# Optimization experiments

Measured on AMD Instinct MI355X. Metric: run time of the kernel, lower is better.

The kernel has to match this reference:

```python
import jax, jax.numpy as jnp
import numpy as np

NUM_HEADS = 8
POOL = 4  # kq_downscale kernel/stride (spatial)
B, S, H, W, C = 32, 8, 32, 32, 128
TOTAL_KEY_DEPTH = 512
VAL_FILTERS = 128
OUT_FILTERS = 64


def _avg_pool(x):
    # tf.nn.avg_pool3d with kernel/stride [1,1,4,4,1], SAME padding (dims divide evenly)
    win = (1, 1, POOL, POOL, 1)
    s = jax.lax.reduce_window(x, 0.0, jax.lax.add, win, win, 'SAME')
    return s / (POOL * POOL)


def _conv2d(x, w, b):
    # TimeDistributed Conv2D, same padding. x: (B,S,H,W,Cin), w: (kh,kw,Cin,Cout)
    Bx, Sx, Hx, Wx, Cx = x.shape
    y = jax.lax.conv_general_dilated(
        x.reshape(Bx * Sx, Hx, Wx, Cx), w, (1, 1), 'SAME',
        dimension_numbers=('NHWC', 'HWIO', 'NHWC'))
    return y.reshape(Bx, Sx, Hx, Wx, -1) + b


def _rel_emb(length_q, length_k, max_rel, table):
    # _generate_relative_positions_embeddings
    rk = jnp.arange(length_k)
    rq = rk[-length_q:]
    idx = jnp.clip(rk[None, :] - rq[:, None], -max_rel, max_rel) + max_rel
    return table[idx]  # (Lq, Lk, depth)


def setup_inputs() -> dict:
    key = jax.random.key(0)
    ks = jax.random.split(key, 11)
    qk_in = (H // POOL) * (W // POOL) * C          # 8*8*128 = 8192
    d_vh = H * W * VAL_FILTERS // NUM_HEADS         # 16384 per-head value depth
    d_kh = TOTAL_KEY_DEPTH // NUM_HEADS             # 64
    return {
        'inputs': jax.random.normal(ks[0], (B, 1, H, W, C), jnp.float32),
        'k_antecedent': jax.random.normal(ks[1], (B, S, H, W, C), jnp.float32),
        'v_antecedent': jax.random.normal(ks[2], (B, S, H, W, C), jnp.float32),
        'w_q': jax.random.normal(ks[3], (qk_in, TOTAL_KEY_DEPTH), jnp.float32) * 0.02,
        'w_k': jax.random.normal(ks[4], (qk_in, TOTAL_KEY_DEPTH), jnp.float32) * 0.02,
        'conv_v_w': jax.random.normal(ks[5], (3, 3, C, VAL_FILTERS), jnp.float32) * 0.02,
        'conv_v_b': jnp.zeros((VAL_FILTERS,), jnp.float32),
        'conv_o_w': jax.random.normal(ks[6], (3, 3, VAL_FILTERS, OUT_FILTERS), jnp.float32) * 0.02,
        'conv_o_b': jnp.zeros((OUT_FILTERS,), jnp.float32),
        'table_k': jax.random.normal(ks[7], (S, d_kh), jnp.float32) * 0.05,
        'table_v': jax.random.normal(ks[8], (S, d_vh), jnp.float32) * 0.05,
    }


def reference(inputs, k_antecedent, v_antecedent, w_q, w_k,
              conv_v_w, conv_v_b, conv_o_w, conv_o_b, table_k, table_v):
    Bx, Sx, Hx, Wx, Cx = v_antecedent.shape
    nh = NUM_HEADS
    max_rel = Sx // 2 - 1  # attn_factor_reduc/2 - 1

    # downscale + flatten q/k antecedents
    q_a = _avg_pool(inputs).reshape(Bx, 1, -1)
    k_a = _avg_pool(k_antecedent).reshape(Bx, Sx, -1)
    q = q_a @ w_q                   # (B,1,Dk)
    k = k_a @ w_k                   # (B,S,Dk)
    v = _conv2d(v_antecedent, conv_v_w, conv_v_b).reshape(Bx, Sx, -1)  # (B,S,Dv)

    def split(x):  # (B,L,D) -> (B,h,L,D/h)
        Bz, L, D = x.shape
        return x.reshape(Bz, L, nh, D // nh).transpose(0, 2, 1, 3)

    q, k, v = split(q), split(k), split(v)
    q = q * (q.shape[-1] ** -0.5)

    # relative-position logits: _relative_attention_inner(q, k, z_k, transpose=True)
    z_k = _rel_emb(1, Sx, max_rel, table_k)  # (1,S,dkh)
    logits = jnp.einsum('bhqd,bhkd->bhqk', q, k) + jnp.einsum('bhqd,qkd->bhqk', q, z_k)
    weights = jax.nn.softmax(logits, axis=-1)  # (B,h,1,S)

    # relative values: _relative_attention_inner(weights, v, z_v, transpose=False)
    z_v = _rel_emb(1, Sx, max_rel, table_v)  # (1,S,dvh)
    x = jnp.einsum('bhqk,bhkd->bhqd', weights, v) + jnp.einsum('bhqk,qkd->bhqd', weights, z_v)

    # combine heads, restore spatial shape, output conv
    x = x.transpose(0, 2, 1, 3).reshape(Bx, 1, Hx, Wx, -1)  # (B,1,H,W,Fv)
    out = _conv2d(x, conv_o_w, conv_o_b)                     # (B,1,H,W,Fo)
    return out
```

## Files before the change

### kernel.cpp

```cpp
#include <hip/hip_runtime.h>
#include <hip/hip_bf16.h>

typedef __hip_bfloat16 bf16;
typedef __attribute__((ext_vector_type(8))) short bf16x8;
typedef __attribute__((ext_vector_type(4))) float f32x4;

constexpr int B_ = 32, S_ = 8, H_ = 32, W_ = 32, C_ = 128;
constexpr int NH_ = 8, KD_ = 512, DKH_ = 64, VF_ = 128, OF_ = 64;
constexpr int QKIN_ = 8192;

static __device__ __forceinline__ short bfbits(float f) {
    bf16 h = __float2bfloat16(f);
    short s;
    __builtin_memcpy(&s, &h, 2);
    return s;
}
static __device__ __forceinline__ unsigned int packbf2(float a, float b) {
    return ((unsigned int)(unsigned short)bfbits(b) << 16) | (unsigned short)bfbits(a);
}


static __device__ __forceinline__ void dev_pool4(const float* __restrict__ in,
                                                 short* __restrict__ out, int idx) {
    int c4 = (idx & 31) * 4;
    int pw = (idx >> 5) & 7;
    int ph = (idx >> 8) & 7;
    int img = idx >> 11;
    const float* p = in + (((size_t)img * H_ + ph * 4) * W_ + pw * 4) * C_ + c4;
    float4 s = {0.f, 0.f, 0.f, 0.f};
#pragma unroll
    for (int half = 0; half < 2; ++half) {
        float4 v[8];
#pragma unroll
        for (int j = 0; j < 8; ++j) {
            int dy = half * 2 + (j >> 2), dx = j & 3;
            v[j] = *reinterpret_cast<const float4*>(p + (dy * W_ + dx) * C_);
        }
#pragma unroll
        for (int j = 0; j < 8; ++j) {
            s.x += v[j].x; s.y += v[j].y; s.z += v[j].z; s.w += v[j].w;
        }
    }
    uint2 pk;
    pk.x = packbf2(s.x * 0.0625f, s.y * 0.0625f);
    pk.y = packbf2(s.z * 0.0625f, s.w * 0.0625f);
    *reinterpret_cast<uint2*>(out + (size_t)img * QKIN_ + (ph * 8 + pw) * 128 + c4) = pk;
}

static __device__ __forceinline__ void dev_wT(const float* __restrict__ w,
                                              short* __restrict__ wT, int local,
                                              float (*t)[65]) {
    int k0 = (local >> 3) * 64, n0 = (local & 7) * 64;
    int c4 = (threadIdx.x & 15) * 4, r16 = threadIdx.x >> 4;
#pragma unroll
    for (int i = 0; i < 4; ++i) {
        int kr = i * 16 + r16;
        float4 v = *reinterpret_cast<const float4*>(
            w + (size_t)(k0 + kr) * KD_ + n0 + c4);
        t[kr][c4 + 0] = v.x;
        t[kr][c4 + 1] = v.y;
        t[kr][c4 + 2] = v.z;
        t[kr][c4 + 3] = v.w;
    }
    __syncthreads();
    int n = threadIdx.x >> 3, kg = threadIdx.x & 7;
#pragma unroll
    for (int half = 0; half < 2; ++half) {
        int nn = n + half * 32;
        short v[8];
#pragma unroll
        for (int j = 0; j < 8; ++j) v[j] = bfbits(t[kg * 8 + j][nn]);
        *reinterpret_cast<bf16x8*>(wT + (size_t)(n0 + nn) * QKIN_ + k0 + kg * 8) =
            *reinterpret_cast<bf16x8*>(v);
    }
}

static __device__ __forceinline__ void dev_wtrans(const float* __restrict__ in,
                                                  short* __restrict__ out, int idx,
                                                  int CO) {
    int tap = idx / (128 * CO);
    int rem = idx % (128 * CO);
    int co = rem / 128;
    int ci = rem & 127;
    out[idx] = bfbits(in[((size_t)tap * 128 + ci) * CO + co]);
}

constexpr int PB_ZERO  = 144;
constexpr int PB_POOLI = PB_ZERO + 256;
constexpr int PB_POOLK = PB_POOLI + 2048;
constexpr int PB_WTQ   = PB_POOLK + 1024;
constexpr int PB_WTK   = PB_WTQ + 1024;
constexpr int PB_WV    = PB_WTK + 576;
constexpr int PB_WO    = PB_WV + 288;

__global__ __launch_bounds__(256) void k_prep(
    const float* __restrict__ inp, const float* __restrict__ k_ant,
    const float* __restrict__ w_q, const float* __restrict__ w_k,
    const float* __restrict__ cvw, const float* __restrict__ cow,
    float* __restrict__ qk_zero, short* __restrict__ q_a, short* __restrict__ k_a,
    short* __restrict__ wqT, short* __restrict__ wkT,
    short* __restrict__ wvT, short* __restrict__ woT) {
    __shared__ float t[64][65];
    int bx = blockIdx.x;
    if (bx < PB_ZERO) {
        int i = (bx * 256 + threadIdx.x) * 4;
        float4 z = {0.f, 0.f, 0.f, 0.f};
        *reinterpret_cast<float4*>(qk_zero + i) = z;
    } else if (bx < PB_POOLI) {
        dev_pool4(inp, q_a, (bx - PB_ZERO) * 256 + threadIdx.x);
    } else if (bx < PB_POOLK) {
        dev_pool4(k_ant, k_a, (bx - PB_POOLI) * 256 + threadIdx.x);
    } else if (bx < PB_WTK) {
        if (bx < PB_WTQ)
            dev_wT(w_q, wqT, bx - PB_POOLK, t);
        else
            dev_wT(w_k, wkT, bx - PB_WTQ, t);
    } else if (bx < PB_WV) {
        dev_wtrans(cvw, wvT, (bx - PB_WTK) * 256 + threadIdx.x, 128);
    } else {
        dev_wtrans(cow, woT, (bx - PB_WV) * 256 + threadIdx.x, 64);
    }
}

__global__ __launch_bounds__(256) void k_gemm2(
    const short* __restrict__ qa, const short* __restrict__ ka,
    const short* __restrict__ wqTp, const short* __restrict__ wkTp,
    float* __restrict__ qo, float* __restrict__ ko) {
    int wave = threadIdx.x >> 6, lane = threadIdx.x & 63;
    int quad = lane >> 4, l15 = lane & 15;
    int id = blockIdx.x;
    const short* A;
    const short* WT;
    float* out;
    int m0, rem;
    if (id < 64) {
        A = qa; WT = wqTp; out = qo; m0 = 0; rem = id;
    } else {
        id -= 64;
        A = ka; WT = wkTp; out = ko;
        m0 = (id >> 6) * 32; rem = id & 63;
    }
    int n0 = (rem & 3) * 128 + wave * 32;
    int k0 = (rem >> 2) * 512;
    f32x4 acc[2][2];
#pragma unroll
    for (int mt = 0; mt < 2; ++mt)
#pragma unroll
        for (int nt = 0; nt < 2; ++nt) acc[mt][nt] = (f32x4){0.f, 0.f, 0.f, 0.f};
    const short* a0p = A + (size_t)(m0 + l15) * QKIN_;
    const short* a1p = a0p + 16 * QKIN_;
    const short* b0p = WT + (size_t)(n0 + l15) * QKIN_;
    const short* b1p = b0p + 16 * QKIN_;
    for (int kk = k0 + quad * 8; kk < k0 + 512; kk += 32) {
        bf16x8 a0 = *reinterpret_cast<const bf16x8*>(a0p + kk);
        bf16x8 a1 = *reinterpret_cast<const bf16x8*>(a1p + kk);
        bf16x8 b0 = *reinterpret_cast<const bf16x8*>(b0p + kk);
        bf16x8 b1 = *reinterpret_cast<const bf16x8*>(b1p + kk);
        acc[0][0] = __builtin_amdgcn_mfma_f32_16x16x32_bf16(a0, b0, acc[0][0], 0, 0, 0);
        acc[0][1] = __builtin_amdgcn_mfma_f32_16x16x32_bf16(a0, b1, acc[0][1], 0, 0, 0);
        acc[1][0] = __builtin_amdgcn_mfma_f32_16x16x32_bf16(a1, b0, acc[1][0], 0, 0, 0);
        acc[1][1] = __builtin_amdgcn_mfma_f32_16x16x32_bf16(a1, b1, acc[1][1], 0, 0, 0);
    }
#pragma unroll
    for (int mt = 0; mt < 2; ++mt)
#pragma unroll
        for (int nt = 0; nt < 2; ++nt)
#pragma unroll
            for (int reg = 0; reg < 4; ++reg)
                atomicAdd(&out[(size_t)(m0 + mt * 16 + quad * 4 + reg) * KD_ +
                               n0 + nt * 16 + l15],
                          acc[mt][nt][reg]);
}

static __device__ __forceinline__ void dev_softmax(
    const float* __restrict__ q, const float* __restrict__ kmat,
    const float* __restrict__ tbk, int b, int h, float* w8s) {
    if (threadIdx.x < 64) {
        int d = threadIdx.x;
        float qv = q[(size_t)b * KD_ + h * DKH_ + d];
        float lg[8];
        float m = -1e30f;
#pragma unroll
        for (int s = 0; s < 8; ++s) {
            int zi = (s < 4) ? 0 : (s - 4);
            float kv = kmat[((size_t)b * S_ + s) * KD_ + h * DKH_ + d] + tbk[zi * DKH_ + d];
            float p = qv * kv * 0.125f;
#pragma unroll
            for (int msk = 1; msk < 64; msk <<= 1) p += __shfl_xor(p, msk);
            lg[s] = p;
            m = fmaxf(m, p);
        }
        float sum = 0.f;
#pragma unroll
        for (int s = 0; s < 8; ++s) {
            lg[s] = expf(lg[s] - m);
            sum += lg[s];
        }
        if (d == 0) {
            float inv = 1.f / sum;
#pragma unroll
            for (int s = 0; s < 8; ++s) w8s[s] = lg[s] * inv;
        }
    }
}

__global__ __launch_bounds__(256) void k_mix(
    const float* __restrict__ v_ant, const float* __restrict__ q,
    const float* __restrict__ kmat, const float* __restrict__ tbk,
    short* __restrict__ xmix) {
    __shared__ float w8s[8];
    int bx = blockIdx.x;
    int b = bx / 48;
    int rem6 = bx % 48;
    int h = rem6 / 6, r = rem6 % 6;
    dev_softmax(q, kmat, tbk, b, h, w8s);
    __syncthreads();
    int yimg = 4 * h - 1 + r;
    short* outp = xmix + ((size_t)(b * 8 + h) * 6 + r) * 4096;
    if (yimg < 0 || yimg >= H_) {
        uint2 z = {0u, 0u};
#pragma unroll
        for (int it = 0; it < 4; ++it) {
            int off = (it * 256 + threadIdx.x) * 4;
            *reinterpret_cast<uint2*>(outp + off) = z;
        }
        return;
    }
    float w8[8];
#pragma unroll
    for (int s = 0; s < 8; ++s) w8[s] = w8s[s];
    const float* base0 = v_ant + (size_t)b * 1048576 + yimg * 4096;
#pragma unroll
    for (int it = 0; it < 4; ++it) {
        int off = (it * 256 + threadIdx.x) * 4;
        float4 v[8];
#pragma unroll
        for (int s = 0; s < 8; ++s)
            v[s] = *reinterpret_cast<const float4*>(base0 + (size_t)s * 131072 + off);
        float4 a = {0.f, 0.f, 0.f, 0.f};
#pragma unroll
        for (int s = 0; s < 8; ++s) {
            a.x = fmaf(w8[s], v[s].x, a.x);
            a.y = fmaf(w8[s], v[s].y, a.y);
            a.z = fmaf(w8[s], v[s].z, a.z);
            a.w = fmaf(w8[s], v[s].w, a.w);
        }
        uint2 pk;
        pk.x = packbf2(a.x, a.y);
        pk.y = packbf2(a.z, a.w);
        *reinterpret_cast<uint2*>(outp + off) = pk;
    }
}

static __device__ __forceinline__ void dev_stage_copy(const short* __restrict__ src,
                                                      short* __restrict__ strip) {
    for (int i = threadIdx.x; i < 384; i += 256) {
        int r = i >> 6, remz = i & 63;
        int side = remz >> 5, cg = remz & 31;
        uint2 z = {0u, 0u};
        *reinterpret_cast<uint2*>(&strip[(r * 34 + side * 33) * 136 + cg * 4]) = z;
    }
#pragma unroll
    for (int round = 0; round < 3; ++round) {
        uint2 vv[8];
#pragma unroll
        for (int j = 0; j < 8; ++j) {
            int i = (round * 8 + j) * 256 + threadIdx.x;
            vv[j] = *reinterpret_cast<const uint2*>(src + i * 4);
        }
#pragma unroll
        for (int j = 0; j < 8; ++j) {
            int i = (round * 8 + j) * 256 + threadIdx.x;
            int r = i >> 10, rem = i & 1023;
            int px = rem >> 5, cg = rem & 31;
            *reinterpret_cast<uint2*>(&strip[(r * 34 + px + 1) * 136 + cg * 4]) = vv[j];
        }
    }
}

static __device__ __forceinline__ void dev_stage6(const short* __restrict__ src,
                                                  int y0, short* __restrict__ strip) {
    for (int i = threadIdx.x; i < 384; i += 256) {
        int r = i >> 6, remz = i & 63;
        int side = remz >> 5, cg = remz & 31;
        uint2 z = {0u, 0u};
        *reinterpret_cast<uint2*>(&strip[(r * 34 + side * 33) * 136 + cg * 4]) = z;
    }
#pragma unroll
    for (int round = 0; round < 3; ++round) {
        uint2 vv[8];
#pragma unroll
        for (int j = 0; j < 8; ++j) {
            int i = (round * 8 + j) * 256 + threadIdx.x;
            int r = i >> 10, rem = i & 1023;
            int yimg = y0 - 1 + r;
            vv[j] = (uint2){0u, 0u};
            if (0 <= yimg && yimg < H_)
                vv[j] = *reinterpret_cast<const uint2*>(src + yimg * 4096 + rem * 4);
        }
#pragma unroll
        for (int j = 0; j < 8; ++j) {
            int i = (round * 8 + j) * 256 + threadIdx.x;
            int r = i >> 10, rem = i & 1023;
            int px = rem >> 5, cg = rem & 31;
            *reinterpret_cast<uint2*>(&strip[(r * 34 + px + 1) * 136 + cg * 4]) = vv[j];
        }
    }
}

__global__ __launch_bounds__(256) void k_convv2(
    const short* __restrict__ xmix, const short* __restrict__ wvT,
    const float* __restrict__ bias, const float* __restrict__ tbv,
    const float* __restrict__ q, const float* __restrict__ kmat,
    const float* __restrict__ tbk, short* __restrict__ x) {
    __shared__ short strip[6 * 34 * 136];
    __shared__ float w8s[8];
    int b = blockIdx.x >> 3, h = blockIdx.x & 7;
    int y0 = 4 * h;
    dev_softmax(q, kmat, tbk, b, h, w8s);
    dev_stage_copy(xmix + (size_t)(b * 8 + h) * 6 * 4096, strip);
    __syncthreads();
    int wave = threadIdx.x >> 6, lane = threadIdx.x & 63;
    int quad = lane >> 4, l15 = lane & 15;
    int n0 = wave * 32;
    f32x4 acc[8][2];
#pragma unroll
    for (int mt = 0; mt < 8; ++mt)
#pragma unroll
        for (int nt = 0; nt < 2; ++nt) acc[mt][nt] = (f32x4){0.f, 0.f, 0.f, 0.f};
    for (int kc = 0; kc < 36; ++kc) {
        int tap = kc >> 2;
        int ci0 = (kc & 3) * 32 + quad * 8;
        int ky = tap / 3, dx = tap % 3;
        bf16x8 bfr[2];
#pragma unroll
        for (int nt = 0; nt < 2; ++nt) {
            int co = n0 + nt * 16 + l15;
            bfr[nt] = *reinterpret_cast<const bf16x8*>(
                wvT + ((size_t)tap * 128 + co) * 128 + ci0);
        }
#pragma unroll
        for (int mt = 0; mt < 8; ++mt) {
            int jout = mt >> 1, half = mt & 1;
            int r = jout + ky;
            int px1 = half * 16 + l15 + dx;
            bf16x8 afr = *reinterpret_cast<const bf16x8*>(
                &strip[(r * 34 + px1) * 136 + ci0]);
            acc[mt][0] = __builtin_amdgcn_mfma_f32_16x16x32_bf16(afr, bfr[0], acc[mt][0], 0, 0, 0);
            acc[mt][1] = __builtin_amdgcn_mfma_f32_16x16x32_bf16(afr, bfr[1], acc[mt][1], 0, 0, 0);
        }
    }
    float cw[4];
    cw[0] = w8s[0] + w8s[1] + w8s[2] + w8s[3] + w8s[4];
    cw[1] = w8s[5];
    cw[2] = w8s[6];
    cw[3] = w8s[7];
#pragma unroll
    for (int mt = 0; mt < 8; ++mt) {
        int jout = mt >> 1, half = mt & 1;
#pragma unroll
        for (int nt = 0; nt < 2; ++nt) {
            int co = n0 + nt * 16 + l15;
            float bv = bias[co];
#pragma unroll
            for (int reg = 0; reg < 4; ++reg) {
                int px = half * 16 + quad * 4 + reg;
                int d = jout * 4096 + px * 128 + co;
                float v = acc[mt][nt][reg] + bv;
                v = fmaf(cw[0], tbv[d], v);
                v = fmaf(cw[1], tbv[16384 + d], v);
                v = fmaf(cw[2], tbv[32768 + d], v);
                v = fmaf(cw[3], tbv[49152 + d], v);
                x[(((size_t)b * H_ + y0 + jout) * W_ + px) * C_ + co] = bfbits(v);
            }
        }
    }
}

__global__ __launch_bounds__(256) void k_convo_mfma(
    const short* __restrict__ x, const short* __restrict__ woT,
    const float* __restrict__ bias, float* __restrict__ out) {
    __shared__ short strip[6 * 34 * 136];
    int b = blockIdx.x >> 3, rg = blockIdx.x & 7;
    int y0 = 4 * rg;
    dev_stage6(x + (size_t)b * 131072, y0, strip);
    __syncthreads();
    int wave = threadIdx.x >> 6, lane = threadIdx.x & 63;
    int quad = lane >> 4, l15 = lane & 15;
    int co = wave * 16 + l15;
    f32x4 acc[8];
#pragma unroll
    for (int mt = 0; mt < 8; ++mt) acc[mt] = (f32x4){0.f, 0.f, 0.f, 0.f};
    for (int kc = 0; kc < 36; ++kc) {
        int tap = kc >> 2;
        int ci0 = (kc & 3) * 32 + quad * 8;
        int ky = tap / 3, dx = tap % 3;
        bf16x8 bfr = *reinterpret_cast<const bf16x8*>(
            woT + ((size_t)tap * 64 + co) * 128 + ci0);
#pragma unroll
        for (int mt = 0; mt < 8; ++mt) {
            int jout = mt >> 1, half = mt & 1;
            int r = jout + ky;
            int px1 = half * 16 + l15 + dx;
            bf16x8 afr = *reinterpret_cast<const bf16x8*>(
                &strip[(r * 34 + px1) * 136 + ci0]);
            acc[mt] = __builtin_amdgcn_mfma_f32_16x16x32_bf16(afr, bfr, acc[mt], 0, 0, 0);
        }
    }
    float bv = bias[co];
#pragma unroll
    for (int mt = 0; mt < 8; ++mt) {
        int jout = mt >> 1, half = mt & 1;
#pragma unroll
        for (int reg = 0; reg < 4; ++reg) {
            int px = half * 16 + quad * 4 + reg;
            out[(((size_t)b * H_ + y0 + jout) * W_ + px) * OF_ + co] = acc[mt][reg] + bv;
        }
    }
}

extern "C" void kernel_launch(void* const* d_in, const int* in_sizes, int n_in,
                              void* d_out, int out_size, void* d_ws, size_t ws_size,
                              hipStream_t stream) {
    const float* inp   = (const float*)d_in[0];
    const float* k_ant = (const float*)d_in[1];
    const float* v_ant = (const float*)d_in[2];
    const float* w_q   = (const float*)d_in[3];
    const float* w_k   = (const float*)d_in[4];
    const float* cvw   = (const float*)d_in[5];
    const float* cvb   = (const float*)d_in[6];
    const float* cow   = (const float*)d_in[7];
    const float* cob   = (const float*)d_in[8];
    const float* tbk   = (const float*)d_in[9];
    const float* tbv   = (const float*)d_in[10];

    char* wsb = (char*)d_ws;
    float* q    = (float*)(wsb + 0);
    float* k    = (float*)(wsb + 65536);
    short* q_a  = (short*)(wsb + 598016);
    short* k_a  = (short*)(wsb + 1122304);
    short* wvT  = (short*)(wsb + 5316608);
    short* woT  = (short*)(wsb + 5611520);
    short* wkT  = (short*)(wsb + 5758976);
    short* wqT  = (short*)(wsb + 14147584);
    short* xmix = (short*)(wsb + 22536192);
    short* x    = wkT;

    k_prep<<<PB_WO, 256, 0, stream>>>(inp, k_ant, w_q, w_k, cvw, cow,
                                      q, q_a, k_a, wqT, wkT, wvT, woT);
    k_gemm2<<<576, 256, 0, stream>>>(q_a, k_a, wqT, wkT, q, k);
    k_mix<<<1536, 256, 0, stream>>>(v_ant, q, k, tbk, xmix);
    k_convv2<<<256, 256, 0, stream>>>(xmix, wvT, cvb, tbv, q, k, tbk, x);
    k_convo_mfma<<<256, 256, 0, stream>>>(x, woT, cob, (float*)d_out);
}
```

Measured before the change: 402.7 us.

## Stage pooling and value-mix loads through LDS with direct global-to-LDS copies

The avg-pool step now has each block copy a full 4-row image strip into shared memory with global_load_lds (16-byte) and then reduce 4x4 windows out of LDS, instead of strided per-thread float4 gathers. k_mix is split into four quarter-row blocks, giving four times as many blocks, and it stages the eight frames through LDS the same way. Softmax is now skipped for padding rows, which only write zeros. The aim is better memory-level parallelism and coalescing in the bandwidth-bound prep and mix stages. The cost is that every mix block recomputes the softmax, and the larger shared-memory footprint (64KB in prep, 32KB in mix) lowers occupancy.

```diff
diff --git a/kernel.cpp b/kernel.cpp
--- a/kernel.cpp
+++ b/kernel.cpp
@@ -19,33 +19,12 @@
     return ((unsigned int)(unsigned short)bfbits(b) << 16) | (unsigned short)bfbits(a);
 }
 
-
-static __device__ __forceinline__ void dev_pool4(const float* __restrict__ in,
-                                                 short* __restrict__ out, int idx) {
-    int c4 = (idx & 31) * 4;
-    int pw = (idx >> 5) & 7;
-    int ph = (idx >> 8) & 7;
-    int img = idx >> 11;
-    const float* p = in + (((size_t)img * H_ + ph * 4) * W_ + pw * 4) * C_ + c4;
-    float4 s = {0.f, 0.f, 0.f, 0.f};
-#pragma unroll
-    for (int half = 0; half < 2; ++half) {
-        float4 v[8];
-#pragma unroll
-        for (int j = 0; j < 8; ++j) {
-            int dy = half * 2 + (j >> 2), dx = j & 3;
-            v[j] = *reinterpret_cast<const float4*>(p + (dy * W_ + dx) * C_);
-        }
-#pragma unroll
-        for (int j = 0; j < 8; ++j) {
-            s.x += v[j].x; s.y += v[j].y; s.z += v[j].z; s.w += v[j].w;
-        }
-    }
-    uint2 pk;
-    pk.x = packbf2(s.x * 0.0625f, s.y * 0.0625f);
-    pk.y = packbf2(s.z * 0.0625f, s.w * 0.0625f);
-    *reinterpret_cast<uint2*>(out + (size_t)img * QKIN_ + (ph * 8 + pw) * 128 + c4) = pk;
-}
+static __device__ __forceinline__ void gl2lds16(const void* g, void* l) {
+    __builtin_amdgcn_global_load_lds(
+        (const __attribute__((address_space(1))) unsigned int*)g,
+        (__attribute__((address_space(3))) unsigned int*)l, 16, 0, 0);
+}
+
 
 static __device__ __forceinline__ void dev_wT(const float* __restrict__ w,
                                               short* __restrict__ wT, int local,
@@ -85,13 +64,12 @@
     out[idx] = bfbits(in[((size_t)tap * 128 + ci) * CO + co]);
 }
 
-constexpr int PB_ZERO  = 144;
-constexpr int PB_POOLI = PB_ZERO + 256;
-constexpr int PB_POOLK = PB_POOLI + 2048;
-constexpr int PB_WTQ   = PB_POOLK + 1024;
-constexpr int PB_WTK   = PB_WTQ + 1024;
-constexpr int PB_WV    = PB_WTK + 576;
-constexpr int PB_WO    = PB_WV + 288;
+constexpr int PB_ZERO = 144;
+constexpr int PB_POOL = PB_ZERO + 2304;
+constexpr int PB_WTQ  = PB_POOL + 1024;
+constexpr int PB_WTK  = PB_WTQ + 1024;
+constexpr int PB_WV   = PB_WTK + 576;
+constexpr int PB_WO   = PB_WV + 288;
 
 __global__ __launch_bounds__(256) void k_prep(
     const float* __restrict__ inp, const float* __restrict__ k_ant,
@@ -100,19 +78,46 @@
     float* __restrict__ qk_zero, short* __restrict__ q_a, short* __restrict__ k_a,
     short* __restrict__ wqT, short* __restrict__ wkT,
     short* __restrict__ wvT, short* __restrict__ woT) {
-    __shared__ float t[64][65];
+    __shared__ float4 smem[4096];
     int bx = blockIdx.x;
     if (bx < PB_ZERO) {
         int i = (bx * 256 + threadIdx.x) * 4;
         float4 z = {0.f, 0.f, 0.f, 0.f};
         *reinterpret_cast<float4*>(qk_zero + i) = z;
-    } else if (bx < PB_POOLI) {
-        dev_pool4(inp, q_a, (bx - PB_ZERO) * 256 + threadIdx.x);
-    } else if (bx < PB_POOLK) {
-        dev_pool4(k_ant, k_a, (bx - PB_POOLI) * 256 + threadIdx.x);
+    } else if (bx < PB_POOL) {
+        int pb = bx - PB_ZERO;
+        int img_g = pb >> 3, ph = pb & 7;
+        const float* src;
+        short* dst;
+        int img;
+        if (img_g < 32) { src = inp;   img = img_g;      dst = q_a; }
+        else            { src = k_ant; img = img_g - 32; dst = k_a; }
+        const float* base = src + ((size_t)img * H_ + ph * 4) * W_ * C_;
+#pragma unroll
+        for (int rnd = 0; rnd < 16; ++rnd) {
+            int i = rnd * 256 + threadIdx.x;
+            gl2lds16(base + (size_t)i * 4,
+                     (char*)smem + ((i >> 6) << 6) * 16);
+        }
+        __syncthreads();
+        int cg = threadIdx.x & 31, pw = threadIdx.x >> 5;
+        float4 s = {0.f, 0.f, 0.f, 0.f};
+#pragma unroll
+        for (int dy = 0; dy < 4; ++dy)
+#pragma unroll
+            for (int dx = 0; dx < 4; ++dx) {
+                float4 v = smem[(dy * 32 + pw * 4 + dx) * 32 + cg];
+                s.x += v.x; s.y += v.y; s.z += v.z; s.w += v.w;
+            }
+        uint2 pk;
+        pk.x = packbf2(s.x * 0.0625f, s.y * 0.0625f);
+        pk.y = packbf2(s.z * 0.0625f, s.w * 0.0625f);
+        *reinterpret_cast<uint2*>(dst + (size_t)img * QKIN_ +
+                                  (ph * 8 + pw) * 128 + cg * 4) = pk;
     } else if (bx < PB_WTK) {
+        float (*t)[65] = (float (*)[65])smem;
         if (bx < PB_WTQ)
-            dev_wT(w_q, wqT, bx - PB_POOLK, t);
+            dev_wT(w_q, wqT, bx - PB_POOL, t);
         else
             dev_wT(w_k, wkT, bx - PB_WTQ, t);
     } else if (bx < PB_WV) {
@@ -208,48 +213,45 @@
     const float* __restrict__ v_ant, const float* __restrict__ q,
     const float* __restrict__ kmat, const float* __restrict__ tbk,
     short* __restrict__ xmix) {
+    __shared__ float4 smem[2048];
     __shared__ float w8s[8];
     int bx = blockIdx.x;
-    int b = bx / 48;
-    int rem6 = bx % 48;
-    int h = rem6 / 6, r = rem6 % 6;
-    dev_softmax(q, kmat, tbk, b, h, w8s);
-    __syncthreads();
+    int qtr = bx & 3;
+    int r = (bx >> 2) % 6;
+    int hb = (bx >> 2) / 6;
+    int h = hb & 7, b = hb >> 3;
     int yimg = 4 * h - 1 + r;
-    short* outp = xmix + ((size_t)(b * 8 + h) * 6 + r) * 4096;
+    short* outp = xmix + ((size_t)hb * 6 + r) * 4096 + qtr * 1024;
     if (yimg < 0 || yimg >= H_) {
         uint2 z = {0u, 0u};
-#pragma unroll
-        for (int it = 0; it < 4; ++it) {
-            int off = (it * 256 + threadIdx.x) * 4;
-            *reinterpret_cast<uint2*>(outp + off) = z;
-        }
+        *reinterpret_cast<uint2*>(outp + threadIdx.x * 4) = z;
         return;
     }
+    dev_softmax(q, kmat, tbk, b, h, w8s);
+    const float* base = v_ant + (size_t)b * 1048576 + yimg * 4096 + qtr * 1024;
+#pragma unroll
+    for (int s = 0; s < 8; ++s) {
+        int i = s * 256 + threadIdx.x;
+        gl2lds16(base + (size_t)s * 131072 + threadIdx.x * 4,
+                 (char*)smem + ((i >> 6) << 6) * 16);
+    }
+    __syncthreads();
     float w8[8];
 #pragma unroll
     for (int s = 0; s < 8; ++s) w8[s] = w8s[s];
-    const float* base0 = v_ant + (size_t)b * 1048576 + yimg * 4096;
-#pragma unroll
-    for (int it = 0; it < 4; ++it) {
-        int off = (it * 256 + threadIdx.x) * 4;
-        float4 v[8];
-#pragma unroll
-        for (int s = 0; s < 8; ++s)
-            v[s] = *reinterpret_cast<const float4*>(base0 + (size_t)s * 131072 + off);
-        float4 a = {0.f, 0.f, 0.f, 0.f};
-#pragma unroll
-        for (int s = 0; s < 8; ++s) {
-            a.x = fmaf(w8[s], v[s].x, a.x);
-            a.y = fmaf(w8[s], v[s].y, a.y);
-            a.z = fmaf(w8[s], v[s].z, a.z);
-            a.w = fmaf(w8[s], v[s].w, a.w);
-        }
-        uint2 pk;
-        pk.x = packbf2(a.x, a.y);
-        pk.y = packbf2(a.z, a.w);
-        *reinterpret_cast<uint2*>(outp + off) = pk;
-    }
+    float4 a = {0.f, 0.f, 0.f, 0.f};
+#pragma unroll
+    for (int s = 0; s < 8; ++s) {
+        float4 v = smem[s * 256 + threadIdx.x];
+        a.x = fmaf(w8[s], v.x, a.x);
+        a.y = fmaf(w8[s], v.y, a.y);
+        a.z = fmaf(w8[s], v.z, a.z);
+        a.w = fmaf(w8[s], v.w, a.w);
+    }
+    uint2 pk;
+    pk.x = packbf2(a.x, a.y);
+    pk.y = packbf2(a.z, a.w);
+    *reinterpret_cast<uint2*>(outp + threadIdx.x * 4) = pk;
 }
 
 static __device__ __forceinline__ void dev_stage_copy(const short* __restrict__ src,
@@ -449,7 +451,7 @@
     k_prep<<<PB_WO, 256, 0, stream>>>(inp, k_ant, w_q, w_k, cvw, cow,
                                       q, q_a, k_a, wqT, wkT, wvT, woT);
     k_gemm2<<<576, 256, 0, stream>>>(q_a, k_a, wqT, wkT, q, k);
-    k_mix<<<1536, 256, 0, stream>>>(v_ant, q, k, tbk, xmix);
+    k_mix<<<6144, 256, 0, stream>>>(v_ant, q, k, tbk, xmix);
     k_convv2<<<256, 256, 0, stream>>>(xmix, wvT, cvb, tbv, q, k, tbk, x);
     k_convo_mfma<<<256, 256, 0, stream>>>(x, woT, cob, (float*)d_out);
 }
```

Result: no change. 395.6 us (-1.8%).
